# Optimization experiments

Hardware: AMD Instinct MI355X
Metric: run time of the kernel (lower is better)

Reference implementation:

```python
import jax, jax.numpy as jnp
import numpy as np

B, S, E, H = 2, 2048, 1024, 16
DH = E // H


def setup_inputs() -> dict:
    key = jax.random.key(0)
    ks = jax.random.split(key, 9)
    s = 1.0 / np.sqrt(E)
    return {
        "queries": jax.random.normal(ks[0], (B, S, E), dtype=jnp.float32),
        "keys": jax.random.normal(ks[1], (B, S, E), dtype=jnp.float32),
        "values": jax.random.normal(ks[2], (B, S, E), dtype=jnp.float32),
        "mask": jax.random.randint(ks[3], (B, 1, 1, S), 0, 2, dtype=jnp.int32),
        "Wq": jax.random.normal(ks[4], (E, E), dtype=jnp.float32) * s,
        "Wk": jax.random.normal(ks[5], (E, E), dtype=jnp.float32) * s,
        "Wv": jax.random.normal(ks[6], (E, E), dtype=jnp.float32) * s,
        "Wo": jax.random.normal(ks[7], (E, E), dtype=jnp.float32) * s,
        "bo": jax.random.normal(ks[8], (E,), dtype=jnp.float32) * s,
    }


def reference(queries, keys, values, mask, Wq, Wk, Wv, Wo, bo):
    n, d_q, _ = queries.shape
    d_k = keys.shape[1]
    # Linear projections (torch Linear: x @ W.T), then split into heads
    q = (queries @ Wq.T).reshape(n, d_q, H, DH)
    k = (keys @ Wk.T).reshape(n, d_k, H, DH)
    v = (values @ Wv.T).reshape(n, d_k, H, DH)
    # [n, H, d_q, d_k] attention scores
    energy = jnp.einsum("nqhd,nkhd->nhqk", q, k)
    energy = jnp.where(mask == 0, jnp.float32(-1e20), energy)
    # NOTE: original scales by sqrt(key seq length), not head dim -- kept faithful
    attn = jax.nn.softmax(energy / jnp.sqrt(jnp.float32(d_k)), axis=3)
    out = jnp.einsum("nhql,nlhd->nqhd", attn, v).reshape(n, d_q, E)
    return out @ Wo.T + bo
```

## Files before the change

kernel.cpp:

```cpp
#include <hip/hip_runtime.h>
#include <hip/hip_bf16.h>

#define BB 2
#define SS 2048
#define EE 1024
#define HH 16
#define DHH 64

using bf16x8 = __attribute__((ext_vector_type(8))) __bf16;
using f32x4  = __attribute__((ext_vector_type(4))) float;

static __device__ __forceinline__ unsigned short f2bf(float f) {
    unsigned int u = __float_as_uint(f);
    u += 0x7FFFu + ((u >> 16) & 1u);
    return (unsigned short)(u >> 16);
}

static __device__ __forceinline__ unsigned int pk2bf(float lo, float hi) {
    union { __hip_bfloat162 h2; unsigned int u; } c;
    c.h2 = __float22bfloat162_rn(float2{lo, hi});
    return c.u;
}

static __device__ __forceinline__ void async_load16(const void* g, void* l) {
    __builtin_amdgcn_global_load_lds(
        (const __attribute__((address_space(1))) unsigned int*)g,
        (__attribute__((address_space(3))) unsigned int*)l, 16, 0, 0);
}

__global__ void cvt_kernel(const float* __restrict__ W0, const float* __restrict__ W1,
                           const float* __restrict__ W2, const float* __restrict__ W3,
                           const float* __restrict__ X0, const float* __restrict__ X1,
                           const float* __restrict__ X2,
                           unsigned short* __restrict__ Wb,
                           unsigned short* __restrict__ D0, unsigned short* __restrict__ D1,
                           unsigned short* __restrict__ D2)
{
    const int z = blockIdx.y;
    const float* src;
    unsigned short* dst;
    if (z < 4) {
        if (blockIdx.x >= 512) return;
        src = (z == 0) ? W0 : (z == 1) ? W1 : (z == 2) ? W2 : W3;
        dst = Wb + (size_t)z * 1048576;
    } else {
        src = (z == 4) ? X0 : (z == 5) ? X1 : X2;
        dst = (z == 4) ? D0 : (z == 5) ? D1 : D2;
    }
    const size_t base = (size_t)blockIdx.x * 2048 + (size_t)threadIdx.x * 8;
    const float4 f0 = *(const float4*)(src + base);
    const float4 f1 = *(const float4*)(src + base + 4);
    uint4 p;
    p.x = pk2bf(f0.x, f0.y); p.y = pk2bf(f0.z, f0.w);
    p.z = pk2bf(f1.x, f1.y); p.w = pk2bf(f1.z, f1.w);
    *(uint4*)(dst + base) = p;
}

template<int MT, bool BF16OUT, bool VT_Z2>
__global__ __launch_bounds__(256, 3)
void gemm_xwt(const unsigned short* __restrict__ X0, const unsigned short* __restrict__ X1,
              const unsigned short* __restrict__ X2,
              const unsigned short* __restrict__ W0, const unsigned short* __restrict__ W1,
              const unsigned short* __restrict__ W2,
              void* __restrict__ Y0, void* __restrict__ Y1, void* __restrict__ Y2,
              const float* __restrict__ bias, int M, int N, int K,
              float s0, float s1, float s2)
{
    constexpr int BK = 32;
    constexpr int NI = MT / 32;
    __shared__ __align__(16) unsigned short As[2][MT * BK];
    __shared__ __align__(16) unsigned short Bs[2][128 * BK];

    const int z = blockIdx.z;
    const unsigned short* __restrict__ X = (z == 0) ? X0 : ((z == 1) ? X1 : X2);
    const unsigned short* __restrict__ W = (z == 0) ? W0 : ((z == 1) ? W1 : W2);
    void* __restrict__ Y                 = (z == 0) ? Y0 : ((z == 1) ? Y1 : Y2);
    const float ysc                      = (z == 0) ? s0 : ((z == 1) ? s1 : s2);

    const int tid  = threadIdx.x;
    const int lane = tid & 63;
    const int wave = tid >> 6;
    const int wm   = (wave >> 1) * (MT / 2);
    const int wn   = (wave & 1) * 64;
    const int m0   = blockIdx.y * MT;
    const int n0   = blockIdx.x * 128;
    const int l16  = lane & 15;
    const int quad = lane >> 4;

    const int arow = lane >> 2;
    const int akc  = (lane & 3) * 8;

    f32x4 acc[NI][4];
    #pragma unroll
    for (int i = 0; i < NI; i++)
        #pragma unroll
        for (int j = 0; j < 4; j++) acc[i][j] = f32x4{0.f, 0.f, 0.f, 0.f};

    auto stage = [&](int k0, int buf) {
        #pragma unroll
        for (int j = 0; j < 2; j++) {
            const int rr = wave * 32 + j * 16;
            async_load16(W + (size_t)(n0 + rr + arow) * K + k0 + akc, Bs[buf] + rr * BK);
        }
        if constexpr (MT == 128) {
            #pragma unroll
            for (int j = 0; j < 2; j++) {
                const int rr = wave * 32 + j * 16;
                async_load16(X + (size_t)(m0 + rr + arow) * K + k0 + akc, As[buf] + rr * BK);
            }
        } else {
            const int rr = wave * 16;
            async_load16(X + (size_t)(m0 + rr + arow) * K + k0 + akc, As[buf] + rr * BK);
        }
    };

    stage(0, 0);
    const int niter = K / BK;
    for (int i = 0; i < niter; i++) {
        const int cur = i & 1;
        __syncthreads();
        if (i + 1 < niter) stage((i + 1) * BK, cur ^ 1);

        bf16x8 afrag[NI], bfrag[4];
        #pragma unroll
        for (int ii = 0; ii < NI; ii++)
            afrag[ii] = *(const bf16x8*)(As[cur] + (wm + ii * 16 + l16) * BK + quad * 8);
        #pragma unroll
        for (int j = 0; j < 4; j++)
            bfrag[j] = *(const bf16x8*)(Bs[cur] + (wn + j * 16 + l16) * BK + quad * 8);
        #pragma unroll
        for (int ii = 0; ii < NI; ii++)
            #pragma unroll
            for (int j = 0; j < 4; j++)
                acc[ii][j] = __builtin_amdgcn_mfma_f32_16x16x32_bf16(afrag[ii], bfrag[j], acc[ii][j], 0, 0, 0);
    }

    if (BF16OUT && VT_Z2 && z == 2) {
        #pragma unroll
        for (int i = 0; i < NI; i++) {
            const int row0 = m0 + wm + i * 16 + quad * 4;
            const int bb   = row0 >> 11;
            const int sx   = row0 & (SS - 1);
            #pragma unroll
            for (int j = 0; j < 4; j++) {
                const int col = n0 + wn + j * 16 + l16;
                uint2 pck;
                pck.x = pk2bf(acc[i][j][0], acc[i][j][1]);
                pck.y = pk2bf(acc[i][j][2], acc[i][j][3]);
                *(uint2*)((unsigned short*)Y + (size_t)(bb * EE + col) * SS + sx) = pck;
            }
        }
    } else {
        #pragma unroll
        for (int i = 0; i < NI; i++) {
            #pragma unroll
            for (int j = 0; j < 4; j++) {
                #pragma unroll
                for (int r = 0; r < 4; r++) {
                    const int row = m0 + wm + i * 16 + quad * 4 + r;
                    const int col = n0 + wn + j * 16 + l16;
                    const float v = acc[i][j][r];
                    if (BF16OUT) {
                        ((unsigned short*)Y)[(size_t)row * N + col] = f2bf(v * ysc);
                    } else {
                        ((float*)Y)[(size_t)row * N + col] = v + bias[col];
                    }
                }
            }
        }
    }
}

__global__ __launch_bounds__(256, 2)
void attn_kernel(const unsigned short* __restrict__ Qb,
                 const unsigned short* __restrict__ Kb,
                 const unsigned short* __restrict__ Vt,
                 const int* __restrict__ mask,
                 unsigned short* __restrict__ AO)
{
    constexpr int LDK = 68;
    constexpr int LDV = 68;
    constexpr int LDP = 68;
    __shared__ __align__(16) unsigned short Ks[64 * LDK];
    __shared__ __align__(16) unsigned short Vs[64 * LDV];
    __shared__ __align__(16) unsigned short Ps[4 * 32 * LDP];
    __shared__ float Msf[64];

    const int tid  = threadIdx.x;
    const int lane = tid & 63;
    const int wave = tid >> 6;
    const int l16  = lane & 15;
    const int quad = lane >> 4;

    const int bh = blockIdx.y;
    const int b  = bh >> 4;
    const int h  = bh & 15;
    const int q0 = blockIdx.x * 128 + wave * 32;

    bf16x8 qf[2][2];
    #pragma unroll
    for (int g = 0; g < 2; g++) {
        const unsigned short* qptr = Qb + (size_t)(b * SS + q0 + g * 16 + l16) * EE + h * DHH;
        qf[g][0] = *(const bf16x8*)(qptr + quad * 8);
        qf[g][1] = *(const bf16x8*)(qptr + 32 + quad * 8);
    }

    float lsum[2] = {0.f, 0.f};
    f32x4 o_acc[2][4];
    #pragma unroll
    for (int g = 0; g < 2; g++)
        #pragma unroll
        for (int j = 0; j < 4; j++) o_acc[g][j] = f32x4{0.f, 0.f, 0.f, 0.f};

    unsigned short* Pw = Ps + wave * 32 * LDP;

    const int srow = tid >> 2;
    const int sc   = (tid & 3) * 16;

    uint4 kr0, kr1, vr0, vr1;
    int   mr = 0;
    auto gload = [&](int t0) {
        const unsigned short* kg = Kb + (size_t)(b * SS + t0 + srow) * EE + h * DHH + sc;
        kr0 = *(const uint4*)(kg);
        kr1 = *(const uint4*)(kg + 8);
        const unsigned short* vg = Vt + (size_t)(b * EE + h * DHH + srow) * SS + t0 + sc;
        vr0 = *(const uint4*)(vg);
        vr1 = *(const uint4*)(vg + 8);
        if (tid < 64) mr = mask[b * SS + t0 + tid];
    };
    gload(0);

    for (int t0 = 0; t0 < SS; t0 += 64) {
        __syncthreads();
        *(uint4*)(Ks + srow * LDK + sc)     = kr0;
        *(uint4*)(Ks + srow * LDK + sc + 8) = kr1;
        *(uint4*)(Vs + srow * LDV + sc)     = vr0;
        *(uint4*)(Vs + srow * LDV + sc + 8) = vr1;
        if (tid < 64) Msf[tid] = (float)mr;
        __syncthreads();

        if (t0 + 64 < SS) gload(t0 + 64);

        #pragma unroll
        for (int nt = 0; nt < 4; nt++) {
            bf16x8 kf0 = *(const bf16x8*)(Ks + (nt * 16 + l16) * LDK + quad * 8);
            bf16x8 kf1 = *(const bf16x8*)(Ks + (nt * 16 + l16) * LDK + 32 + quad * 8);
            const f32x4 mf = *(const f32x4*)(Msf + nt * 16 + quad * 4);
            #pragma unroll
            for (int g = 0; g < 2; g++) {
                f32x4 a = f32x4{0.f, 0.f, 0.f, 0.f};
                a = __builtin_amdgcn_mfma_f32_16x16x32_bf16(kf0, qf[g][0], a, 0, 0, 0);
                a = __builtin_amdgcn_mfma_f32_16x16x32_bf16(kf1, qf[g][1], a, 0, 0, 0);
                float p0 = __expf(a[0]) * mf[0];
                float p1 = __expf(a[1]) * mf[1];
                float p2 = __expf(a[2]) * mf[2];
                float p3 = __expf(a[3]) * mf[3];
                lsum[g] += (p0 + p1) + (p2 + p3);
                uint2 pck;
                pck.x = pk2bf(p0, p1);
                pck.y = pk2bf(p2, p3);
                *(uint2*)(Pw + (g * 16 + l16) * LDP + nt * 16 + quad * 4) = pck;
            }
        }

        __builtin_amdgcn_s_waitcnt(0xC07F);

        #pragma unroll
        for (int s2 = 0; s2 < 2; s2++) {
            bf16x8 pf0 = *(const bf16x8*)(Pw + l16 * LDP + s2 * 32 + quad * 8);
            bf16x8 pf1 = *(const bf16x8*)(Pw + (16 + l16) * LDP + s2 * 32 + quad * 8);
            #pragma unroll
            for (int jg = 0; jg < 4; jg++) {
                bf16x8 vf = *(const bf16x8*)(Vs + (jg * 16 + l16) * LDV + s2 * 32 + quad * 8);
                o_acc[0][jg] = __builtin_amdgcn_mfma_f32_16x16x32_bf16(vf, pf0, o_acc[0][jg], 0, 0, 0);
                o_acc[1][jg] = __builtin_amdgcn_mfma_f32_16x16x32_bf16(vf, pf1, o_acc[1][jg], 0, 0, 0);
            }
        }
    }

    #pragma unroll
    for (int g = 0; g < 2; g++) {
        float ls = lsum[g];
        ls += __shfl_xor(ls, 16, 64);
        ls += __shfl_xor(ls, 32, 64);
        const float rl = 1.0f / ls;
        const size_t orow = (size_t)(b * SS + q0 + g * 16 + l16) * EE + h * DHH;
        #pragma unroll
        for (int jg = 0; jg < 4; jg++) {
            uint2 pck;
            pck.x = pk2bf(o_acc[g][jg][0] * rl, o_acc[g][jg][1] * rl);
            pck.y = pk2bf(o_acc[g][jg][2] * rl, o_acc[g][jg][3] * rl);
            *(uint2*)(AO + orow + jg * 16 + quad * 4) = pck;
        }
    }
}

extern "C" void kernel_launch(void* const* d_in, const int* in_sizes, int n_in,
                              void* d_out, int out_size, void* d_ws, size_t ws_size,
                              hipStream_t stream)
{
    (void)in_sizes; (void)n_in; (void)out_size; (void)ws_size;
    const float* queries = (const float*)d_in[0];
    const float* keys    = (const float*)d_in[1];
    const float* values  = (const float*)d_in[2];
    const int*   mask    = (const int*)d_in[3];
    const float* Wq      = (const float*)d_in[4];
    const float* Wk      = (const float*)d_in[5];
    const float* Wv      = (const float*)d_in[6];
    const float* Wo      = (const float*)d_in[7];
    const float* bo      = (const float*)d_in[8];

    const size_t NE = (size_t)BB * SS * EE;
    const size_t WE = (size_t)EE * EE;

    unsigned short* Xq  = (unsigned short*)d_out;
    unsigned short* Xk  = Xq + NE;
    unsigned short* Wb  = (unsigned short*)d_ws;
    unsigned short* Xv  = Wb + 4 * WE;
    unsigned short* Qb  = Xv + NE;
    unsigned short* Kb  = Qb + NE;
    unsigned short* Vtb = Kb + NE;
    unsigned short* AOb = Xv;

    const int M = BB * SS, N = EE, K = EE;
    const float qscale = 0.022097086912079608f;

    cvt_kernel<<<dim3(2048, 7), 256, 0, stream>>>(
        Wq, Wk, Wv, Wo, queries, keys, values, Wb, Xq, Xk, Xv);

    dim3 gproj(N / 128, M / 128, 3);
    gemm_xwt<128, true, true><<<gproj, 256, 0, stream>>>(
        Xq, Xk, Xv, Wb, Wb + WE, Wb + 2 * WE,
        (void*)Qb, (void*)Kb, (void*)Vtb, nullptr, M, N, K,
        qscale, 1.0f, 1.0f);

    attn_kernel<<<dim3(SS / 128, BB * HH), 256, 0, stream>>>(Qb, Kb, Vtb, mask, AOb);

    dim3 gout(N / 128, M / 64, 1);
    gemm_xwt<64, false, false><<<gout, 256, 0, stream>>>(
        AOb, AOb, AOb, Wb + 3 * WE, Wb + 3 * WE, Wb + 3 * WE,
        d_out, d_out, d_out, bo, M, N, K, 1.0f, 1.0f, 1.0f);
}
```

Before: 248.0 us.

## Shrink attention blocks, fold mask into exp2 bias, and tile output GEMM 64x64

The attention kernel now runs 128-thread blocks covering 32 queries, with 16 queries per wave. This gives 4x more blocks, aiming for better occupancy and load balance. The mask is now added as a -150 bias in the MFMA accumulator init, and exp is replaced by exp2 with log2e folded into the Q scale, which removes a multiply per score. The output projection GEMM uses 64x64 tiles so it launches more blocks. In exchange, each K/V tile is reused across fewer queries, so global and LDS traffic per FLOP rises, and masked keys now get exp2(-150+s) instead of an exact zero.

Result: slower. 485.1 us (+95.6%).

```diff
diff --git a/kernel.cpp b/kernel.cpp
--- a/kernel.cpp
+++ b/kernel.cpp
@@ -9,6 +9,12 @@
 
 using bf16x8 = __attribute__((ext_vector_type(8))) __bf16;
 using f32x4  = __attribute__((ext_vector_type(4))) float;
+
+#if __has_builtin(__builtin_amdgcn_exp2f)
+#define EXP2(x) __builtin_amdgcn_exp2f(x)
+#else
+#define EXP2(x) __exp2f(x)
+#endif
 
 static __device__ __forceinline__ unsigned short f2bf(float f) {
     unsigned int u = __float_as_uint(f);
@@ -56,7 +62,7 @@
     *(uint4*)(dst + base) = p;
 }
 
-template<int MT, bool BF16OUT, bool VT_Z2>
+template<int MT, int NT, bool BF16OUT, bool VT_Z2>
 __global__ __launch_bounds__(256, 3)
 void gemm_xwt(const unsigned short* __restrict__ X0, const unsigned short* __restrict__ X1,
               const unsigned short* __restrict__ X2,
@@ -68,8 +74,9 @@
 {
     constexpr int BK = 32;
     constexpr int NI = MT / 32;
+    constexpr int NJ = NT / 32;
     __shared__ __align__(16) unsigned short As[2][MT * BK];
-    __shared__ __align__(16) unsigned short Bs[2][128 * BK];
+    __shared__ __align__(16) unsigned short Bs[2][NT * BK];
 
     const int z = blockIdx.z;
     const unsigned short* __restrict__ X = (z == 0) ? X0 : ((z == 1) ? X1 : X2);
@@ -81,35 +88,30 @@
     const int lane = tid & 63;
     const int wave = tid >> 6;
     const int wm   = (wave >> 1) * (MT / 2);
-    const int wn   = (wave & 1) * 64;
+    const int wn   = (wave & 1) * (NT / 2);
     const int m0   = blockIdx.y * MT;
-    const int n0   = blockIdx.x * 128;
+    const int n0   = blockIdx.x * NT;
     const int l16  = lane & 15;
     const int quad = lane >> 4;
 
     const int arow = lane >> 2;
     const int akc  = (lane & 3) * 8;
 
-    f32x4 acc[NI][4];
+    f32x4 acc[NI][NJ];
     #pragma unroll
     for (int i = 0; i < NI; i++)
         #pragma unroll
-        for (int j = 0; j < 4; j++) acc[i][j] = f32x4{0.f, 0.f, 0.f, 0.f};
+        for (int j = 0; j < NJ; j++) acc[i][j] = f32x4{0.f, 0.f, 0.f, 0.f};
 
     auto stage = [&](int k0, int buf) {
         #pragma unroll
-        for (int j = 0; j < 2; j++) {
-            const int rr = wave * 32 + j * 16;
+        for (int j = 0; j < NT / 64; j++) {
+            const int rr = wave * (NT / 4) + j * 16;
             async_load16(W + (size_t)(n0 + rr + arow) * K + k0 + akc, Bs[buf] + rr * BK);
         }
-        if constexpr (MT == 128) {
-            #pragma unroll
-            for (int j = 0; j < 2; j++) {
-                const int rr = wave * 32 + j * 16;
-                async_load16(X + (size_t)(m0 + rr + arow) * K + k0 + akc, As[buf] + rr * BK);
-            }
-        } else {
-            const int rr = wave * 16;
+        #pragma unroll
+        for (int j = 0; j < MT / 64; j++) {
+            const int rr = wave * (MT / 4) + j * 16;
             async_load16(X + (size_t)(m0 + rr + arow) * K + k0 + akc, As[buf] + rr * BK);
         }
     };
@@ -121,17 +123,17 @@
         __syncthreads();
         if (i + 1 < niter) stage((i + 1) * BK, cur ^ 1);
 
-        bf16x8 afrag[NI], bfrag[4];
+        bf16x8 afrag[NI], bfrag[NJ];
         #pragma unroll
         for (int ii = 0; ii < NI; ii++)
             afrag[ii] = *(const bf16x8*)(As[cur] + (wm + ii * 16 + l16) * BK + quad * 8);
         #pragma unroll
-        for (int j = 0; j < 4; j++)
+        for (int j = 0; j < NJ; j++)
             bfrag[j] = *(const bf16x8*)(Bs[cur] + (wn + j * 16 + l16) * BK + quad * 8);
         #pragma unroll
         for (int ii = 0; ii < NI; ii++)
             #pragma unroll
-            for (int j = 0; j < 4; j++)
+            for (int j = 0; j < NJ; j++)
                 acc[ii][j] = __builtin_amdgcn_mfma_f32_16x16x32_bf16(afrag[ii], bfrag[j], acc[ii][j], 0, 0, 0);
     }
 
@@ -142,7 +144,7 @@
             const int bb   = row0 >> 11;
             const int sx   = row0 & (SS - 1);
             #pragma unroll
-            for (int j = 0; j < 4; j++) {
+            for (int j = 0; j < NJ; j++) {
                 const int col = n0 + wn + j * 16 + l16;
                 uint2 pck;
                 pck.x = pk2bf(acc[i][j][0], acc[i][j][1]);
@@ -154,7 +156,7 @@
         #pragma unroll
         for (int i = 0; i < NI; i++) {
             #pragma unroll
-            for (int j = 0; j < 4; j++) {
+            for (int j = 0; j < NJ; j++) {
                 #pragma unroll
                 for (int r = 0; r < 4; r++) {
                     const int row = m0 + wm + i * 16 + quad * 4 + r;
@@ -171,7 +173,7 @@
     }
 }
 
-__global__ __launch_bounds__(256, 2)
+__global__ __launch_bounds__(128, 4)
 void attn_kernel(const unsigned short* __restrict__ Qb,
                  const unsigned short* __restrict__ Kb,
                  const unsigned short* __restrict__ Vt,
@@ -183,8 +185,8 @@
     constexpr int LDP = 68;
     __shared__ __align__(16) unsigned short Ks[64 * LDK];
     __shared__ __align__(16) unsigned short Vs[64 * LDV];
-    __shared__ __align__(16) unsigned short Ps[4 * 32 * LDP];
-    __shared__ float Msf[64];
+    __shared__ __align__(16) unsigned short Ps[2 * 16 * LDP];
+    __shared__ __align__(16) float Msf[64];
 
     const int tid  = threadIdx.x;
     const int lane = tid & 63;
@@ -195,48 +197,47 @@
     const int bh = blockIdx.y;
     const int b  = bh >> 4;
     const int h  = bh & 15;
-    const int q0 = blockIdx.x * 128 + wave * 32;
-
-    bf16x8 qf[2][2];
+    const int q0 = blockIdx.x * 32 + wave * 16;
+
+    bf16x8 qf[2];
+    {
+        const unsigned short* qptr = Qb + (size_t)(b * SS + q0 + l16) * EE + h * DHH;
+        qf[0] = *(const bf16x8*)(qptr + quad * 8);
+        qf[1] = *(const bf16x8*)(qptr + 32 + quad * 8);
+    }
+
+    float lsum = 0.f;
+    f32x4 o_acc[4];
     #pragma unroll
-    for (int g = 0; g < 2; g++) {
-        const unsigned short* qptr = Qb + (size_t)(b * SS + q0 + g * 16 + l16) * EE + h * DHH;
-        qf[g][0] = *(const bf16x8*)(qptr + quad * 8);
-        qf[g][1] = *(const bf16x8*)(qptr + 32 + quad * 8);
-    }
-
-    float lsum[2] = {0.f, 0.f};
-    f32x4 o_acc[2][4];
-    #pragma unroll
-    for (int g = 0; g < 2; g++)
-        #pragma unroll
-        for (int j = 0; j < 4; j++) o_acc[g][j] = f32x4{0.f, 0.f, 0.f, 0.f};
-
-    unsigned short* Pw = Ps + wave * 32 * LDP;
-
-    const int srow = tid >> 2;
-    const int sc   = (tid & 3) * 16;
-
-    uint4 kr0, kr1, vr0, vr1;
+    for (int j = 0; j < 4; j++) o_acc[j] = f32x4{0.f, 0.f, 0.f, 0.f};
+
+    unsigned short* Pw = Ps + wave * 16 * LDP;
+
+    const int srow = tid >> 1;
+    const int sc   = (tid & 1) * 32;
+
+    uint4 kr[4], vr[4];
     int   mr = 0;
     auto gload = [&](int t0) {
         const unsigned short* kg = Kb + (size_t)(b * SS + t0 + srow) * EE + h * DHH + sc;
-        kr0 = *(const uint4*)(kg);
-        kr1 = *(const uint4*)(kg + 8);
         const unsigned short* vg = Vt + (size_t)(b * EE + h * DHH + srow) * SS + t0 + sc;
-        vr0 = *(const uint4*)(vg);
-        vr1 = *(const uint4*)(vg + 8);
+        #pragma unroll
+        for (int j = 0; j < 4; j++) {
+            kr[j] = *(const uint4*)(kg + j * 8);
+            vr[j] = *(const uint4*)(vg + j * 8);
+        }
         if (tid < 64) mr = mask[b * SS + t0 + tid];
     };
     gload(0);
 
     for (int t0 = 0; t0 < SS; t0 += 64) {
         __syncthreads();
-        *(uint4*)(Ks + srow * LDK + sc)     = kr0;
-        *(uint4*)(Ks + srow * LDK + sc + 8) = kr1;
-        *(uint4*)(Vs + srow * LDV + sc)     = vr0;
-        *(uint4*)(Vs + srow * LDV + sc + 8) = vr1;
-        if (tid < 64) Msf[tid] = (float)mr;
+        #pragma unroll
+        for (int j = 0; j < 4; j++) {
+            *(uint4*)(Ks + srow * LDK + sc + j * 8) = kr[j];
+            *(uint4*)(Vs + srow * LDV + sc + j * 8) = vr[j];
+        }
+        if (tid < 64) Msf[tid] = mr ? 0.0f : -150.0f;
         __syncthreads();
 
         if (t0 + 64 < SS) gload(t0 + 64);
@@ -245,53 +246,44 @@
         for (int nt = 0; nt < 4; nt++) {
             bf16x8 kf0 = *(const bf16x8*)(Ks + (nt * 16 + l16) * LDK + quad * 8);
             bf16x8 kf1 = *(const bf16x8*)(Ks + (nt * 16 + l16) * LDK + 32 + quad * 8);
-            const f32x4 mf = *(const f32x4*)(Msf + nt * 16 + quad * 4);
-            #pragma unroll
-            for (int g = 0; g < 2; g++) {
-                f32x4 a = f32x4{0.f, 0.f, 0.f, 0.f};
-                a = __builtin_amdgcn_mfma_f32_16x16x32_bf16(kf0, qf[g][0], a, 0, 0, 0);
-                a = __builtin_amdgcn_mfma_f32_16x16x32_bf16(kf1, qf[g][1], a, 0, 0, 0);
-                float p0 = __expf(a[0]) * mf[0];
-                float p1 = __expf(a[1]) * mf[1];
-                float p2 = __expf(a[2]) * mf[2];
-                float p3 = __expf(a[3]) * mf[3];
-                lsum[g] += (p0 + p1) + (p2 + p3);
-                uint2 pck;
-                pck.x = pk2bf(p0, p1);
-                pck.y = pk2bf(p2, p3);
-                *(uint2*)(Pw + (g * 16 + l16) * LDP + nt * 16 + quad * 4) = pck;
-            }
+            const f32x4 cinit = *(const f32x4*)(Msf + nt * 16 + quad * 4);
+            f32x4 a = __builtin_amdgcn_mfma_f32_16x16x32_bf16(kf0, qf[0], cinit, 0, 0, 0);
+            a = __builtin_amdgcn_mfma_f32_16x16x32_bf16(kf1, qf[1], a, 0, 0, 0);
+            const float p0 = EXP2(a[0]);
+            const float p1 = EXP2(a[1]);
+            const float p2 = EXP2(a[2]);
+            const float p3 = EXP2(a[3]);
+            lsum += (p0 + p1) + (p2 + p3);
+            uint2 pck;
+            pck.x = pk2bf(p0, p1);
+            pck.y = pk2bf(p2, p3);
+            *(uint2*)(Pw + l16 * LDP + nt * 16 + quad * 4) = pck;
         }
 
         __builtin_amdgcn_s_waitcnt(0xC07F);
 
         #pragma unroll
         for (int s2 = 0; s2 < 2; s2++) {
-            bf16x8 pf0 = *(const bf16x8*)(Pw + l16 * LDP + s2 * 32 + quad * 8);
-            bf16x8 pf1 = *(const bf16x8*)(Pw + (16 + l16) * LDP + s2 * 32 + quad * 8);
+            bf16x8 pf = *(const bf16x8*)(Pw + l16 * LDP + s2 * 32 + quad * 8);
             #pragma unroll
             for (int jg = 0; jg < 4; jg++) {
                 bf16x8 vf = *(const bf16x8*)(Vs + (jg * 16 + l16) * LDV + s2 * 32 + quad * 8);
-                o_acc[0][jg] = __builtin_amdgcn_mfma_f32_16x16x32_bf16(vf, pf0, o_acc[0][jg], 0, 0, 0);
-                o_acc[1][jg] = __builtin_amdgcn_mfma_f32_16x16x32_bf16(vf, pf1, o_acc[1][jg], 0, 0, 0);
+                o_acc[jg] = __builtin_amdgcn_mfma_f32_16x16x32_bf16(vf, pf, o_acc[jg], 0, 0, 0);
             }
         }
     }
 
+    lsum += __shfl_xor(lsum, 16, 64);
+    lsum += __shfl_xor(lsum, 32, 64);
+    const float rl = 1.0f / lsum;
+
+    const size_t orow = (size_t)(b * SS + q0 + l16) * EE + h * DHH;
     #pragma unroll
-    for (int g = 0; g < 2; g++) {
-        float ls = lsum[g];
-        ls += __shfl_xor(ls, 16, 64);
-        ls += __shfl_xor(ls, 32, 64);
-        const float rl = 1.0f / ls;
-        const size_t orow = (size_t)(b * SS + q0 + g * 16 + l16) * EE + h * DHH;
-        #pragma unroll
-        for (int jg = 0; jg < 4; jg++) {
-            uint2 pck;
-            pck.x = pk2bf(o_acc[g][jg][0] * rl, o_acc[g][jg][1] * rl);
-            pck.y = pk2bf(o_acc[g][jg][2] * rl, o_acc[g][jg][3] * rl);
-            *(uint2*)(AO + orow + jg * 16 + quad * 4) = pck;
-        }
+    for (int jg = 0; jg < 4; jg++) {
+        uint2 pck;
+        pck.x = pk2bf(o_acc[jg][0] * rl, o_acc[jg][1] * rl);
+        pck.y = pk2bf(o_acc[jg][2] * rl, o_acc[jg][3] * rl);
+        *(uint2*)(AO + orow + jg * 16 + quad * 4) = pck;
     }
 }
 
@@ -323,21 +315,21 @@
     unsigned short* AOb = Xv;
 
     const int M = BB * SS, N = EE, K = EE;
-    const float qscale = 0.022097086912079608f;
+    const float qscale = 0.022097086912079608f * 1.4426950408889634f;
 
     cvt_kernel<<<dim3(2048, 7), 256, 0, stream>>>(
         Wq, Wk, Wv, Wo, queries, keys, values, Wb, Xq, Xk, Xv);
 
     dim3 gproj(N / 128, M / 128, 3);
-    gemm_xwt<128, true, true><<<gproj, 256, 0, stream>>>(
+    gemm_xwt<128, 128, true, true><<<gproj, 256, 0, stream>>>(
         Xq, Xk, Xv, Wb, Wb + WE, Wb + 2 * WE,
         (void*)Qb, (void*)Kb, (void*)Vtb, nullptr, M, N, K,
         qscale, 1.0f, 1.0f);
 
-    attn_kernel<<<dim3(SS / 128, BB * HH), 256, 0, stream>>>(Qb, Kb, Vtb, mask, AOb);
-
-    dim3 gout(N / 128, M / 64, 1);
-    gemm_xwt<64, false, false><<<gout, 256, 0, stream>>>(
+    attn_kernel<<<dim3(SS / 32, BB * HH), 128, 0, stream>>>(Qb, Kb, Vtb, mask, AOb);
+
+    dim3 gout(N / 64, M / 64, 1);
+    gemm_xwt<64, 64, false, false><<<gout, 256, 0, stream>>>(
         AOb, AOb, AOb, Wb + 3 * WE, Wb + 3 * WE, Wb + 3 * WE,
         d_out, d_out, d_out, bo, M, N, K, 1.0f, 1.0f, 1.0f);
 }
```
